# Performance work log

Measured on AMD Instinct MI355X. Metric: run time of the kernel, lower is better.

## Reference

```python
import jax, jax.numpy as jnp
import numpy as np

Q_MAX = 127.0  # int8 activation quant range
NIB_MASK = 15  # 4-bit mask


def setup_inputs() -> dict:
    key = jax.random.key(0)
    k1, k2, k3, k4, k5 = jax.random.split(key, 5)
    M, IN, OUT = 4096, 4096, 11008
    x = jax.random.normal(k1, (M, IN), dtype=jnp.float32)
    # packed int4 weights: two nibbles per byte, [OUT, IN//2]
    qweight = jax.random.randint(k2, (OUT, IN // 2), 0, 256, dtype=jnp.int32)
    qzeros = jax.random.randint(k3, (OUT, 1), 0, 16, dtype=jnp.int32)
    scales = jax.random.uniform(k4, (OUT, 1), dtype=jnp.float32) * 0.01 + 1e-4
    bias = jax.random.normal(k5, (OUT,), dtype=jnp.float32) * 0.01
    clampv = jnp.full((1,), 3.0, dtype=jnp.float32)
    return {"x": x, "qweight": qweight, "qzeros": qzeros,
            "scales": scales, "bias": bias, "clampv": clampv}


def _unpack_int4(qweight, qzeros, scales):
    # high nibble -> even position, low nibble -> odd position (matches torch unpack)
    hi = (qweight >> 4) & NIB_MASK          # [OUT, IN//2]
    lo = qweight & NIB_MASK                 # [OUT, IN//2]
    intw = jnp.stack([hi, lo], axis=-1).reshape(qweight.shape[0], -1)  # [OUT, IN]
    return (intw - qzeros).astype(scales.dtype) * scales               # [OUT, IN]


def reference(x, qweight, qzeros, scales, bias, clampv):
    cv = clampv[0]
    # static activation fake-quant at scale clampv/127 (quantize_activation_static)
    x = jnp.clip(x, -cv, cv)
    a_scale = cv / Q_MAX
    qx = jnp.clip(jnp.round(x / a_scale), -Q_MAX, Q_MAX) * a_scale
    # dequantize packed int4 weights, then GEMM
    W = _unpack_int4(qweight, qzeros, scales)   # [OUT, IN]
    out = qx @ W.T + bias[None, :]              # [M, OUT]
    return out
```

## Files before the change

### kernel.cpp

```cpp
#include <hip/hip_runtime.h>
#include <stdint.h>

typedef int v4i __attribute__((ext_vector_type(4)));

static constexpr int Mdim = 4096;
static constexpr int Kdim = 4096;
static constexpr int Ndim = 11008;

#define BM 256
#define BN 256
#define BK 128
#define NT (Kdim / BK)

__device__ __forceinline__ void gload_lds16(const void* gp, void* lp) {
  __builtin_amdgcn_global_load_lds((const __attribute__((address_space(1))) void*)gp,
                                   (__attribute__((address_space(3))) void*)lp,
                                   16, 0, 0);
}

__global__ void k_quant(const float* __restrict__ x, const float* __restrict__ clampv,
                        signed char* __restrict__ qa, int* __restrict__ rowsum) {
  const int row = blockIdx.x;
  const int t = threadIdx.x;
  const float cv = clampv[0];
  const float a_scale = cv / 127.0f;
  const float4* xp = (const float4*)(x + (size_t)row * Kdim) + t * 4;
  int s = 0;
  int w[4];
#pragma unroll
  for (int i = 0; i < 4; ++i) {
    float4 f = xp[i];
    float q0 = fminf(fmaxf(rintf(fminf(fmaxf(f.x, -cv), cv) / a_scale), -127.f), 127.f);
    float q1 = fminf(fmaxf(rintf(fminf(fmaxf(f.y, -cv), cv) / a_scale), -127.f), 127.f);
    float q2 = fminf(fmaxf(rintf(fminf(fmaxf(f.z, -cv), cv) / a_scale), -127.f), 127.f);
    float q3 = fminf(fmaxf(rintf(fminf(fmaxf(f.w, -cv), cv) / a_scale), -127.f), 127.f);
    int i0 = (int)q0, i1 = (int)q1, i2 = (int)q2, i3 = (int)q3;
    s += i0 + i1 + i2 + i3;
    w[i] = (i0 & 255) | ((i1 & 255) << 8) | ((i2 & 255) << 16) | ((i3 & 255) << 24);
  }
  ((int4*)(qa + (size_t)row * Kdim))[t] = make_int4(w[0], w[1], w[2], w[3]);
#pragma unroll
  for (int off = 32; off > 0; off >>= 1) s += __shfl_down(s, off, 64);
  __shared__ int red[4];
  if ((t & 63) == 0) red[t >> 6] = s;
  __syncthreads();
  if (t == 0) rowsum[row] = red[0] + red[1] + red[2] + red[3];
}

__global__ void k_unpack(const int4* __restrict__ qw, uint2* __restrict__ wb) {
  const int idx = blockIdx.x * 256 + threadIdx.x;
  int4 q = qw[idx];
  uint2 r;
  r.x = (unsigned)(((q.x >> 4) & 15) | ((q.x & 15) << 8) |
                   (((q.y >> 4) & 15) << 16) | ((q.y & 15) << 24));
  r.y = (unsigned)(((q.z >> 4) & 15) | ((q.z & 15) << 8) |
                   (((q.w >> 4) & 15) << 16) | ((q.w & 15) << 24));
  wb[idx] = r;
}

__global__ __launch_bounds__(512, 2) void k_gemm(
    const signed char* __restrict__ A, const signed char* __restrict__ B,
    const float* __restrict__ scales, const int* __restrict__ qzeros,
    const float* __restrict__ bias, const float* __restrict__ clampv,
    const int* __restrict__ rowsum, float* __restrict__ out) {
  __shared__ signed char lds[131072];
  signed char* As = lds;
  signed char* Bs = lds + 65536;

  const int t = threadIdx.x;
  const int lane = t & 63;
  const int wave = t >> 6;
  const int wm = (wave >> 2) * 128;
  const int wn = (wave & 3) * 64;

  const int bid = blockIdx.x;
  const int swz = (bid & 7) * 86 + (bid >> 3);
  const int mt = swz / 43;
  const int nt = swz - mt * 43;
  const int m0 = mt * BM;
  const int n0 = nt * BN;

  const int srow = t >> 3;
  const int sch = (t & 7) ^ (srow & 7);
  const signed char* gA = A + (size_t)(m0 + srow) * Kdim + sch * 16;
  const signed char* gB = B + (size_t)(n0 + srow) * Kdim + sch * 16;
  const int sdst = t * 16;

#define STAGE_A(buf, k0)                                               \
  {                                                                    \
    _Pragma("unroll") for (int i = 0; i < 4; ++i)                      \
        gload_lds16(gA + (size_t)(i * 64) * Kdim + (k0),               \
                    As + (buf) * 32768 + i * 8192 + sdst);             \
  }
#define STAGE_B(buf, k0)                                               \
  {                                                                    \
    _Pragma("unroll") for (int i = 0; i < 4; ++i)                      \
        gload_lds16(gB + (size_t)(i * 64) * Kdim + (k0),               \
                    Bs + (buf) * 32768 + i * 8192 + sdst);             \
  }

  const int col = lane & 15;
  const int q16 = lane >> 4;
  const int c7 = col & 7;
  int aoff[2], boff[2];
#pragma unroll
  for (int ks = 0; ks < 2; ++ks) {
    const int pos = ((ks * 4 + q16) ^ c7) * 16;
    aoff[ks] = (wm + col) * BK + pos;
    boff[ks] = (wn + col) * BK + pos;
  }

  v4i acc[8][4] = {};
  v4i a[2][8], b[2][4];

#define LOADK(bank, ks_)                                                    \
  {                                                                         \
    _Pragma("unroll") for (int i = 0; i < 8; ++i)                           \
        a[bank][i] = *(const v4i*)(Ac + i * 2048 + aoff[ks_]);              \
    _Pragma("unroll") for (int j = 0; j < 4; ++j)                           \
        b[bank][j] = *(const v4i*)(Bc + j * 2048 + boff[ks_]);              \
  }
#define MFMAK(bank)                                                         \
  {                                                                         \
    __builtin_amdgcn_s_setprio(1);                                          \
    _Pragma("unroll") for (int i = 0; i < 8; ++i)                           \
        _Pragma("unroll") for (int j = 0; j < 4; ++j)                       \
            acc[i][j] = __builtin_amdgcn_mfma_i32_16x16x64_i8(              \
                a[bank][i], b[bank][j], acc[i][j], 0, 0, 0);                \
    __builtin_amdgcn_s_setprio(0);                                          \
  }

  STAGE_A(0, 0);
  STAGE_B(0, 0);
  asm volatile("s_waitcnt vmcnt(0)" ::: "memory");
  __builtin_amdgcn_s_barrier();

  int cur = 0;
  for (int ti = 0; ti < NT - 1; ++ti) {
    const int nk = (ti + 1) * BK;
    const signed char* Ac = As + cur * 32768;
    const signed char* Bc = Bs + cur * 32768;

    STAGE_A(cur ^ 1, nk);
    STAGE_B(cur ^ 1, nk);

    LOADK(0, 0);
    LOADK(1, 1);
    MFMAK(0);
    MFMAK(1);

    asm volatile("s_waitcnt vmcnt(0)" ::: "memory");
    __builtin_amdgcn_s_barrier();
    cur ^= 1;
  }
  {
    const signed char* Ac = As + cur * 32768;
    const signed char* Bc = Bs + cur * 32768;
    LOADK(0, 0);
    LOADK(1, 1);
    MFMAK(0);
    MFMAK(1);
  }
#undef STAGE_A
#undef STAGE_B
#undef LOADK
#undef MFMAK

  const float a_scale = clampv[0] / 127.0f;
  const int rq = q16 * 4;
  int rs[8][4];
#pragma unroll
  for (int i = 0; i < 8; ++i)
#pragma unroll
    for (int r = 0; r < 4; ++r)
      rs[i][r] = rowsum[m0 + wm + i * 16 + rq + r];
#pragma unroll
  for (int j = 0; j < 4; ++j) {
    const int n = n0 + wn + j * 16 + col;
    const float sn = scales[n] * a_scale;
    const int zn = qzeros[n];
    const float bn = bias[n];
#pragma unroll
    for (int i = 0; i < 8; ++i) {
      const int mb = m0 + wm + i * 16 + rq;
#pragma unroll
      for (int r = 0; r < 4; ++r) {
        const int iv = acc[i][j][r] - zn * rs[i][r];
        out[(size_t)(mb + r) * Ndim + n] = (float)iv * sn + bn;
      }
    }
  }
}

extern "C" void kernel_launch(void* const* d_in, const int* in_sizes, int n_in,
                              void* d_out, int out_size, void* d_ws, size_t ws_size,
                              hipStream_t stream) {
  const float* x  = (const float*)d_in[0];
  const int* qw   = (const int*)d_in[1];
  const int* qz   = (const int*)d_in[2];
  const float* sc = (const float*)d_in[3];
  const float* bi = (const float*)d_in[4];
  const float* cv = (const float*)d_in[5];
  float* out = (float*)d_out;

  signed char* qa = (signed char*)d_ws;
  signed char* wb = qa + (size_t)Mdim * Kdim;
  int* rowsum = (int*)(wb + (size_t)Ndim * Kdim);

  k_quant<<<Mdim, 256, 0, stream>>>(x, cv, qa, rowsum);
  k_unpack<<<(Ndim * (Kdim / 2) / 4) / 256, 256, 0, stream>>>((const int4*)qw, (uint2*)wb);
  k_gemm<<<dim3((Mdim / BM) * (Ndim / BN)), 512, 0, stream>>>(qa, wb, sc, qz, bi, cv, rowsum, out);
}
```

Baseline: 462.4 us.

## Split K-tile MFMA into four phases with interleaved LDS loads and barriers

Restructures the inner loop so each K tile runs as four quadrant phases. Each phase loads only the A/B fragments it needs from LDS, hits a workgroup barrier, then issues 16 MFMAs. This halves fragment register usage (16 v4i instead of 24) and staggers LDS reads against MFMA work across waves, in the style of a ping-pong schedule. The cost is four extra barriers per K iteration, which could stall waves and serialise the compute.

```diff
diff --git a/kernel.cpp b/kernel.cpp
--- a/kernel.cpp
+++ b/kernel.cpp
@@ -111,22 +111,53 @@
   }
 
   v4i acc[8][4] = {};
-  v4i a[2][8], b[2][4];
-
-#define LOADK(bank, ks_)                                                    \
+  v4i a0[4], a1[4], b0[4], b1[4];
+
+#define PHASE_TILE()                                                        \
   {                                                                         \
-    _Pragma("unroll") for (int i = 0; i < 8; ++i)                           \
-        a[bank][i] = *(const v4i*)(Ac + i * 2048 + aoff[ks_]);              \
+                   \
     _Pragma("unroll") for (int j = 0; j < 4; ++j)                           \
-        b[bank][j] = *(const v4i*)(Bc + j * 2048 + boff[ks_]);              \
-  }
-#define MFMAK(bank)                                                         \
-  {                                                                         \
-    __builtin_amdgcn_s_setprio(1);                                          \
-    _Pragma("unroll") for (int i = 0; i < 8; ++i)                           \
+        b0[j] = *(const v4i*)(Bc + j * 2048 + boff[0]);                     \
+    _Pragma("unroll") for (int i = 0; i < 4; ++i)                           \
+        a0[i] = *(const v4i*)(Ac + i * 2048 + aoff[0]);                     \
+    __builtin_amdgcn_s_barrier();                                           \
+    __builtin_amdgcn_s_setprio(1);                                          \
+    _Pragma("unroll") for (int i = 0; i < 4; ++i)                           \
         _Pragma("unroll") for (int j = 0; j < 4; ++j)                       \
             acc[i][j] = __builtin_amdgcn_mfma_i32_16x16x64_i8(              \
-                a[bank][i], b[bank][j], acc[i][j], 0, 0, 0);                \
+                a0[i], b0[j], acc[i][j], 0, 0, 0);                          \
+    __builtin_amdgcn_s_setprio(0);                                          \
+                   \
+    _Pragma("unroll") for (int i = 0; i < 4; ++i)                           \
+        a1[i] = *(const v4i*)(Ac + (i + 4) * 2048 + aoff[0]);               \
+    _Pragma("unroll") for (int j = 0; j < 4; ++j)                           \
+        b1[j] = *(const v4i*)(Bc + j * 2048 + boff[1]);                     \
+    __builtin_amdgcn_s_barrier();                                           \
+    __builtin_amdgcn_s_setprio(1);                                          \
+    _Pragma("unroll") for (int i = 0; i < 4; ++i)                           \
+        _Pragma("unroll") for (int j = 0; j < 4; ++j)                       \
+            acc[i + 4][j] = __builtin_amdgcn_mfma_i32_16x16x64_i8(          \
+                a1[i], b0[j], acc[i + 4][j], 0, 0, 0);                      \
+    __builtin_amdgcn_s_setprio(0);                                          \
+                          \
+    _Pragma("unroll") for (int i = 0; i < 4; ++i)                           \
+        a0[i] = *(const v4i*)(Ac + i * 2048 + aoff[1]);                     \
+    __builtin_amdgcn_s_barrier();                                           \
+    __builtin_amdgcn_s_setprio(1);                                          \
+    _Pragma("unroll") for (int i = 0; i < 4; ++i)                           \
+        _Pragma("unroll") for (int j = 0; j < 4; ++j)                       \
+            acc[i][j] = __builtin_amdgcn_mfma_i32_16x16x64_i8(              \
+                a0[i], b1[j], acc[i][j], 0, 0, 0);                          \
+    __builtin_amdgcn_s_setprio(0);                                          \
+                          \
+    _Pragma("unroll") for (int i = 0; i < 4; ++i)                           \
+        a1[i] = *(const v4i*)(Ac + (i + 4) * 2048 + aoff[1]);               \
+    __builtin_amdgcn_s_barrier();                                           \
+    __builtin_amdgcn_s_setprio(1);                                          \
+    _Pragma("unroll") for (int i = 0; i < 4; ++i)                           \
+        _Pragma("unroll") for (int j = 0; j < 4; ++j)                       \
+            acc[i + 4][j] = __builtin_amdgcn_mfma_i32_16x16x64_i8(          \
+                a1[i], b1[j], acc[i + 4][j], 0, 0, 0);                      \
     __builtin_amdgcn_s_setprio(0);                                          \
   }
 
@@ -144,10 +175,7 @@
     STAGE_A(cur ^ 1, nk);
     STAGE_B(cur ^ 1, nk);
 
-    LOADK(0, 0);
-    LOADK(1, 1);
-    MFMAK(0);
-    MFMAK(1);
+    PHASE_TILE();
 
     asm volatile("s_waitcnt vmcnt(0)" ::: "memory");
     __builtin_amdgcn_s_barrier();
@@ -156,15 +184,11 @@
   {
     const signed char* Ac = As + cur * 32768;
     const signed char* Bc = Bs + cur * 32768;
-    LOADK(0, 0);
-    LOADK(1, 1);
-    MFMAK(0);
-    MFMAK(1);
+    PHASE_TILE();
   }
 #undef STAGE_A
 #undef STAGE_B
-#undef LOADK
-#undef MFMAK
+#undef PHASE_TILE
 
   const float a_scale = clampv[0] / 127.0f;
   const int rq = q16 * 4;
```

Result: slower. 479.5 us (+3.7%).

## Load B fragments directly from global into registers, dropping B LDS staging

Applied to the files above, without the earlier changes.

Removes the LDS double-buffer for the weight tile and has each wave read its B MFMA operands straight from global memory each K step. This halves LDS usage, which may allow more blocks per CU and cuts LDS traffic and barrier work for B. In exchange, the global loads are issued in the same iteration they are consumed, so their latency is exposed. The two waves that share a column slice also fetch the same data twice through the caches.

```diff
diff --git a/kernel.cpp b/kernel.cpp
--- a/kernel.cpp
+++ b/kernel.cpp
@@ -63,9 +63,7 @@
     const float* __restrict__ scales, const int* __restrict__ qzeros,
     const float* __restrict__ bias, const float* __restrict__ clampv,
     const int* __restrict__ rowsum, float* __restrict__ out) {
-  __shared__ signed char lds[131072];
-  signed char* As = lds;
-  signed char* Bs = lds + 65536;
+  __shared__ signed char As[65536];
 
   const int t = threadIdx.x;
   const int lane = t & 63;
@@ -83,42 +81,39 @@
   const int srow = t >> 3;
   const int sch = (t & 7) ^ (srow & 7);
   const signed char* gA = A + (size_t)(m0 + srow) * Kdim + sch * 16;
-  const signed char* gB = B + (size_t)(n0 + srow) * Kdim + sch * 16;
   const int sdst = t * 16;
 
 #define STAGE_A(buf, k0)                                               \
   {                                                                    \
     _Pragma("unroll") for (int i = 0; i < 4; ++i)                      \
         gload_lds16(gA + (size_t)(i * 64) * Kdim + (k0),               \
-                    As + (buf) * 32768 + i * 8192 + sdst);             \
-  }
-#define STAGE_B(buf, k0)                                               \
-  {                                                                    \
-    _Pragma("unroll") for (int i = 0; i < 4; ++i)                      \
-        gload_lds16(gB + (size_t)(i * 64) * Kdim + (k0),               \
-                    Bs + (buf) * 32768 + i * 8192 + sdst);             \
+                    &As[(buf) * 32768 + i * 8192 + sdst]);             \
   }
 
   const int col = lane & 15;
   const int q16 = lane >> 4;
   const int c7 = col & 7;
-  int aoff[2], boff[2];
-#pragma unroll
-  for (int ks = 0; ks < 2; ++ks) {
-    const int pos = ((ks * 4 + q16) ^ c7) * 16;
-    aoff[ks] = (wm + col) * BK + pos;
-    boff[ks] = (wn + col) * BK + pos;
-  }
+  int aoff[2];
+#pragma unroll
+  for (int ks = 0; ks < 2; ++ks)
+    aoff[ks] = (wm + col) * BK + (((ks * 4 + q16) ^ c7) * 16);
+
+  const signed char* gBf = B + (size_t)(n0 + wn + col) * Kdim + q16 * 16;
 
   v4i acc[8][4] = {};
   v4i a[2][8], b[2][4];
 
-#define LOADK(bank, ks_)                                                    \
+#define LOADB(k0)                                                           \
+  {                                                                         \
+    _Pragma("unroll") for (int ks = 0; ks < 2; ++ks)                        \
+        _Pragma("unroll") for (int j = 0; j < 4; ++j)                       \
+            b[ks][j] = *(const v4i*)(gBf + (size_t)(j * 16) * Kdim +        \
+                                     (k0) + ks * 64);                       \
+  }
+#define LOADA(bank, ks_)                                                    \
   {                                                                         \
     _Pragma("unroll") for (int i = 0; i < 8; ++i)                           \
         a[bank][i] = *(const v4i*)(Ac + i * 2048 + aoff[ks_]);              \
-    _Pragma("unroll") for (int j = 0; j < 4; ++j)                           \
-        b[bank][j] = *(const v4i*)(Bc + j * 2048 + boff[ks_]);              \
   }
 #define MFMAK(bank)                                                         \
   {                                                                         \
@@ -131,21 +126,18 @@
   }
 
   STAGE_A(0, 0);
-  STAGE_B(0, 0);
   asm volatile("s_waitcnt vmcnt(0)" ::: "memory");
   __builtin_amdgcn_s_barrier();
 
   int cur = 0;
   for (int ti = 0; ti < NT - 1; ++ti) {
-    const int nk = (ti + 1) * BK;
-    const signed char* Ac = As + cur * 32768;
-    const signed char* Bc = Bs + cur * 32768;
-
-    STAGE_A(cur ^ 1, nk);
-    STAGE_B(cur ^ 1, nk);
-
-    LOADK(0, 0);
-    LOADK(1, 1);
+    const int k0 = ti * BK;
+    const signed char* Ac = &As[cur * 32768];
+
+    STAGE_A(cur ^ 1, k0 + BK);
+    LOADB(k0);
+    LOADA(0, 0);
+    LOADA(1, 1);
     MFMAK(0);
     MFMAK(1);
 
@@ -154,16 +146,17 @@
     cur ^= 1;
   }
   {
-    const signed char* Ac = As + cur * 32768;
-    const signed char* Bc = Bs + cur * 32768;
-    LOADK(0, 0);
-    LOADK(1, 1);
+    const int k0 = (NT - 1) * BK;
+    const signed char* Ac = &As[cur * 32768];
+    LOADB(k0);
+    LOADA(0, 0);
+    LOADA(1, 1);
     MFMAK(0);
     MFMAK(1);
   }
 #undef STAGE_A
-#undef STAGE_B
-#undef LOADK
+#undef LOADB
+#undef LOADA
 #undef MFMAK
 
   const float a_scale = clampv[0] / 127.0f;
```

Result: slower. 587.9 us (+27.1%).
